# Performance work log

Measured on AMD Instinct MI355X. Metric: run time of the kernel, lower is better.

The kernel has to match this reference:

```python
import jax, jax.numpy as jnp
import numpy as np

B, T, D = 64, 4096, 100   # batch, tokens, token_dim == code_dim
K = 4                     # discrete_size: codebook entries
BETA = 0.25               # commitment loss weight


def setup_inputs() -> dict:
    key = jax.random.key(0)
    k_x, k_w, k_b, k_c = jax.random.split(key, 4)
    x = jax.random.normal(k_x, (B, T, D), dtype=jnp.float32)
    W1 = jax.random.normal(k_w, (D, D), dtype=jnp.float32) * (1.0 / np.sqrt(D))
    b1 = jax.random.normal(k_b, (D,), dtype=jnp.float32) * 0.01
    codebook = jax.random.normal(k_c, (K, D), dtype=jnp.float32)
    return {"x": x, "W1": W1, "b1": b1, "codebook": codebook, "quantize": 1}


def reference(x, W1, b1, codebook, quantize):
    # Linear1: Linear(100,100) + ReLU (torch Linear: x @ W.T + b)
    h = jax.nn.relu(jnp.einsum("btd,ed->bte", x, W1) + b1)  # [B,T,D]
    if not quantize:
        return (h, 0, 0, 0)
    # quantizer.compress: VQ-style cdist/argmin/straight-through/loss
    flat = h.reshape(-1, D)  # [N,D]
    d2 = (jnp.sum(flat * flat, axis=-1, keepdims=True)
          - 2.0 * flat @ codebook.T
          + jnp.sum(codebook * codebook, axis=-1))
    idx = jnp.argmin(d2, axis=-1)          # [N] nearest code indices
    q = codebook[idx]                       # [N,D] gathered codes
    sg = jax.lax.stop_gradient
    # codebook loss + commitment loss
    vq_loss = (jnp.mean((sg(flat) - q) ** 2)
               + BETA * jnp.mean((flat - sg(q)) ** 2))
    # straight-through quantized output
    aux = (flat + sg(q - flat)).reshape(B, T, D)
    payload = idx.reshape(B, T)
    return (h, payload, aux, vq_loss)
```

## Files before the change

### kernel.cpp

```cpp
#include <hip/hip_runtime.h>

#define D_DIM   100
#define K_CODES 4
#define RPB     64
#define TPB     256
#define PITCH   65
#define N_ROWS  262144
#define KP      128
#define NP      128
#define TAU     0.25
#define GRID_GEMM 1024
#define NTILES  4

typedef __attribute__((ext_vector_type(8))) __bf16 bf16x8;
typedef __attribute__((ext_vector_type(4))) float  f32x4;

__device__ __forceinline__ unsigned short f2bf_rne(float f) {
    unsigned int u = __builtin_bit_cast(unsigned int, f);
    unsigned int r = u + 0x7fffu + ((u >> 16) & 1u);
    return (unsigned short)(r >> 16);
}
__device__ __forceinline__ float bf2f(unsigned short b) {
    unsigned int u = ((unsigned int)b) << 16;
    return __builtin_bit_cast(float, u);
}
__device__ __forceinline__ void load_lds16(const float* g, float* s) {
    __builtin_amdgcn_global_load_lds(
        (const __attribute__((address_space(1))) unsigned int*)g,
        (__attribute__((address_space(3))) unsigned int*)s, 16, 0, 0);
}
__device__ __forceinline__ void stage_x(const float* xg, float* s, int wave, int lane) {
    #pragma unroll
    for (int it = 0; it < 6; ++it) {
        int cbase = it * 256 + wave * 64;
        load_lds16(xg + (size_t)(cbase + lane) * 4, s + cbase * 4);
    }
    if (wave == 0) load_lds16(xg + (size_t)(1536 + lane) * 4, s + 1536 * 4);
}

__device__ __forceinline__ void bar_lgkm() {
    __builtin_amdgcn_sched_barrier(0);
    asm volatile("s_waitcnt lgkmcnt(0)" ::: "memory");
    __builtin_amdgcn_s_barrier();
    __builtin_amdgcn_sched_barrier(0);
}
__device__ __forceinline__ void bar_vm() {
    __builtin_amdgcn_sched_barrier(0);
    asm volatile("s_waitcnt vmcnt(0) lgkmcnt(0)" ::: "memory");
    __builtin_amdgcn_s_barrier();
    __builtin_amdgcn_sched_barrier(0);
}

__global__ __launch_bounds__(256) void split_w_kernel(
    const float* __restrict__ W1,
    unsigned short* __restrict__ Whi, unsigned short* __restrict__ Wlo)
{
    int i = blockIdx.x * 256 + threadIdx.x;
    if (i >= NP * KP) return;
    int n = i / KP, k = i % KP;
    float w = (n < D_DIM && k < D_DIM) ? W1[n * D_DIM + k] : 0.0f;
    unsigned short hb = f2bf_rne(w);
    float lo = w - bf2f(hb);
    Whi[i] = hb;
    Wlo[i] = f2bf_rne(lo);
}

__global__ __launch_bounds__(TPB, 4) void gemm_relu_mfma(
    const float* __restrict__ x,
    const unsigned short* __restrict__ Whi, const unsigned short* __restrict__ Wlo,
    const float* __restrict__ b1, float* __restrict__ out_h)
{
    __shared__ __align__(16) float buf0[6500];
    __shared__ __align__(16) float buf1[6500];
    const int tid  = threadIdx.x;
    const int lane = tid & 63;
    const int wave = tid >> 6;

    const int bcol0 = wave * 32;
    const int bn  = lane & 15;
    const int bk  = (lane >> 4) * 8;
    bf16x8 bh[2][4], bl[2][4];
    #pragma unroll
    for (int ct = 0; ct < 2; ++ct) {
        int n = bcol0 + ct * 16 + bn;
        #pragma unroll
        for (int kt = 0; kt < 4; ++kt) {
            int off = n * KP + kt * 32 + bk;
            bh[ct][kt] = *reinterpret_cast<const bf16x8*>(Whi + off);
            bl[ct][kt] = *reinterpret_cast<const bf16x8*>(Wlo + off);
        }
    }
    float bias[2];
    #pragma unroll
    for (int ct = 0; ct < 2; ++ct) {
        int n = bcol0 + ct * 16 + bn;
        bias[ct] = (n < D_DIM) ? b1[n] : 0.0f;
    }
    if (tid < 32) { buf0[6400 + tid] = 0.0f; buf1[6400 + tid] = 0.0f; }
    stage_x(x + (size_t)blockIdx.x * RPB * D_DIM, buf0, wave, lane);

    const int am = lane & 15;
    const int ak = (lane >> 4) * 8;

    for (int it = 0; it < NTILES; ++it) {
        const int tile = blockIdx.x + it * GRID_GEMM;
        const int rowBase = tile * RPB;
        float* cur = (it & 1) ? buf1 : buf0;
        float* nxt = (it & 1) ? buf0 : buf1;

        bar_vm();

        if (it + 1 < NTILES)
            stage_x(x + (size_t)(blockIdx.x + (it + 1) * GRID_GEMM) * RPB * D_DIM,
                    nxt, wave, lane);

        f32x4 acc[4][2];
        #pragma unroll
        for (int rt = 0; rt < 4; ++rt) {
            acc[rt][0] = (f32x4){0.f, 0.f, 0.f, 0.f};
            acc[rt][1] = (f32x4){0.f, 0.f, 0.f, 0.f};
        }
        #pragma unroll
        for (int rt = 0; rt < 4; ++rt) {
            const int rbase = (rt * 16 + am) * D_DIM;
            #pragma unroll
            for (int kt = 0; kt < 4; ++kt) {
                const float* p = cur + rbase + kt * 32 + ak;
                f32x4 f0 = *reinterpret_cast<const f32x4*>(p);
                f32x4 f1 = *reinterpret_cast<const f32x4*>(p + 4);
                bf16x8 ah, al;
                #pragma unroll
                for (int i = 0; i < 4; ++i) {
                    __bf16 h0 = (__bf16)f0[i];
                    ah[i] = h0;
                    al[i] = (__bf16)(f0[i] - (float)h0);
                    __bf16 h1 = (__bf16)f1[i];
                    ah[4 + i] = h1;
                    al[4 + i] = (__bf16)(f1[i] - (float)h1);
                }
                acc[rt][0] = __builtin_amdgcn_mfma_f32_16x16x32_bf16(ah, bl[0][kt], acc[rt][0], 0, 0, 0);
                acc[rt][0] = __builtin_amdgcn_mfma_f32_16x16x32_bf16(al, bh[0][kt], acc[rt][0], 0, 0, 0);
                acc[rt][0] = __builtin_amdgcn_mfma_f32_16x16x32_bf16(ah, bh[0][kt], acc[rt][0], 0, 0, 0);
                acc[rt][1] = __builtin_amdgcn_mfma_f32_16x16x32_bf16(ah, bl[1][kt], acc[rt][1], 0, 0, 0);
                acc[rt][1] = __builtin_amdgcn_mfma_f32_16x16x32_bf16(al, bh[1][kt], acc[rt][1], 0, 0, 0);
                acc[rt][1] = __builtin_amdgcn_mfma_f32_16x16x32_bf16(ah, bh[1][kt], acc[rt][1], 0, 0, 0);
            }
        }
        bar_lgkm();

        #pragma unroll
        for (int rt = 0; rt < 4; ++rt) {
            int rb = rt * 16 + (lane >> 4) * 4;
            #pragma unroll
            for (int ct = 0; ct < 2; ++ct) {
                int n = bcol0 + ct * 16 + bn;
                if (n < D_DIM) {
                    #pragma unroll
                    for (int i = 0; i < 4; ++i)
                        cur[n * PITCH + rb + i] = fmaxf(acc[rt][ct][i] + bias[ct], 0.0f);
                }
            }
        }
        bar_lgkm();

        float* hg = out_h + (size_t)rowBase * D_DIM;
        for (int v = tid; v < RPB * 25; v += TPB) {
            int r = v / 25;
            int d = (v % 25) * 4;
            reinterpret_cast<float4*>(hg)[v] = make_float4(
                cur[d * PITCH + r], cur[(d + 1) * PITCH + r],
                cur[(d + 2) * PITCH + r], cur[(d + 3) * PITCH + r]);
        }
    }
}

__global__ __launch_bounds__(TPB) void vq_kernel(
    const float* __restrict__ h, const float* __restrict__ x,
    const float* __restrict__ W1, const float* __restrict__ b1,
    const float* __restrict__ cb, const int* __restrict__ qflag,
    float* __restrict__ out_pay, float* __restrict__ out_aux,
    double* __restrict__ partials)
{
    __shared__ float  tile[D_DIM][PITCH];
    __shared__ double d2s[K_CODES][RPB];
    __shared__ int    idxs[RPB];
    __shared__ unsigned long long flagmask;
    const int tid  = threadIdx.x;
    const int lane = tid & 63;
    const int wave = tid >> 6;
    const int blk  = blockIdx.x;
    const int rowBase = blk * RPB;
    const int qz = *qflag;

    if (qz) {
        const float* hgc = h + (size_t)rowBase * D_DIM;
        for (int v = tid; v < (RPB * D_DIM) / 4; v += TPB) {
            float4 val = reinterpret_cast<const float4*>(hgc)[v];
            int r = v / 25;
            int d = (v % 25) * 4;
            tile[d + 0][r] = val.x; tile[d + 1][r] = val.y;
            tile[d + 2][r] = val.z; tile[d + 3][r] = val.w;
        }
        __syncthreads();
        {
            const int k = __builtin_amdgcn_readfirstlane(wave & 3);
            const float* crow = cb + k * D_DIM;
            double s = 0.0;
            #pragma unroll
            for (int d = 0; d < D_DIM; ++d) {
                double dh = (double)tile[d][lane] - (double)crow[d];
                s = fma(dh, dh, s);
            }
            d2s[k][lane] = s;
        }
        __syncthreads();

        if (wave == 0) {
            double best = d2s[0][lane], second = 1e300;
            int bi = 0;
            #pragma unroll
            for (int k = 1; k < K_CODES; ++k) {
                double v = d2s[k][lane];
                if (v < best) { second = best; best = v; bi = k; }
                else if (v < second) { second = v; }
            }
            idxs[lane] = bi;
            unsigned long long m = __ballot((second - best) < TAU);
            if (lane == 0) flagmask = m;
        }
        __syncthreads();

        {
            unsigned long long m = flagmask;
            int i = 0;
            while (m) {
                int r = __ffsll((long long)m) - 1;
                m &= m - 1;
                if ((i & 3) == wave) {
                    const int e1 = lane;
                    const int e2 = 64 + lane;
                    const bool has2 = (e2 < D_DIM);
                    float z1 = b1[e1];
                    float z2 = has2 ? b1[e2] : 0.0f;
                    const float* xr  = x + (size_t)(rowBase + r) * D_DIM;
                    const float* w1r = W1 + e1 * D_DIM;
                    const float* w2r = W1 + (has2 ? e2 : 0) * D_DIM;
                    #pragma unroll
                    for (int d4 = 0; d4 < 25; ++d4) {
                        float4 xv = reinterpret_cast<const float4*>(xr)[d4];
                        float4 wa = reinterpret_cast<const float4*>(w1r)[d4];
                        z1 = fmaf(xv.x, wa.x, z1); z1 = fmaf(xv.y, wa.y, z1);
                        z1 = fmaf(xv.z, wa.z, z1); z1 = fmaf(xv.w, wa.w, z1);
                        float4 wb = reinterpret_cast<const float4*>(w2r)[d4];
                        z2 = fmaf(xv.x, wb.x, z2); z2 = fmaf(xv.y, wb.y, z2);
                        z2 = fmaf(xv.z, wb.z, z2); z2 = fmaf(xv.w, wb.w, z2);
                    }
                    float h1 = fmaxf(z1, 0.0f);
                    float h2 = fmaxf(z2, 0.0f);
                    double dk[K_CODES];
                    #pragma unroll
                    for (int k = 0; k < K_CODES; ++k) {
                        double p;
                        {
                            double dh = (double)h1 - (double)cb[k * D_DIM + e1];
                            p = dh * dh;
                        }
                        if (has2) {
                            double dh = (double)h2 - (double)cb[k * D_DIM + e2];
                            p = fma(dh, dh, p);
                        }
                        for (int off = 32; off > 0; off >>= 1)
                            p += __shfl_down(p, off);
                        dk[k] = p;
                    }
                    if (lane == 0) {
                        double best = dk[0];
                        int bi = 0;
                        #pragma unroll
                        for (int k = 1; k < K_CODES; ++k)
                            if (dk[k] < best) { best = dk[k]; bi = k; }
                        idxs[r] = bi;
                    }
                }
                ++i;
            }
        }
        __syncthreads();

        if (wave == 0) {
            int bi = idxs[lane];
            out_pay[rowBase + lane] = (float)bi;
            double d2min = d2s[bi][lane];
            for (int off = 32; off > 0; off >>= 1)
                d2min += __shfl_down(d2min, off);
            if (lane == 0) partials[blk] = d2min;
        }

        float* ag = out_aux + (size_t)rowBase * D_DIM;
        for (int v = tid; v < (RPB * D_DIM) / 4; v += TPB) {
            int r = v / 25;
            int d = (v % 25) * 4;
            int bi = idxs[r];
            reinterpret_cast<float4*>(ag)[v] =
                reinterpret_cast<const float4*>(cb + bi * D_DIM + d)[0];
        }
    } else {
        if (wave == 0) {
            out_pay[rowBase + lane] = 0.0f;
            if (lane == 0) partials[blk] = 0.0;
        }
        float* ag = out_aux + (size_t)rowBase * D_DIM;
        for (int v = tid; v < (RPB * D_DIM) / 4; v += TPB)
            reinterpret_cast<float4*>(ag)[v] = make_float4(0, 0, 0, 0);
    }
}

__global__ __launch_bounds__(256) void vq_final_kernel(
    const double* __restrict__ partials, int n, float* __restrict__ loss_out)
{
    __shared__ double sm[256];
    int tid = threadIdx.x;
    double s = 0.0;
    for (int i = tid; i < n; i += 256) s += partials[i];
    sm[tid] = s;
    __syncthreads();
    for (int off = 128; off > 0; off >>= 1) {
        if (tid < off) sm[tid] += sm[tid + off];
        __syncthreads();
    }
    if (tid == 0) {
        double mse = sm[0] / ((double)N_ROWS * (double)D_DIM);
        loss_out[0] = (float)(1.25 * mse);
    }
}

extern "C" void kernel_launch(void* const* d_in, const int* in_sizes, int n_in,
                              void* d_out, int out_size, void* d_ws, size_t ws_size,
                              hipStream_t stream) {
    const float* x  = (const float*)d_in[0];
    const float* W1 = (const float*)d_in[1];
    const float* b1 = (const float*)d_in[2];
    const float* cb = (const float*)d_in[3];
    const int* qflag = (const int*)d_in[4];

    float* out = (float*)d_out;
    const int NR = in_sizes[0] / D_DIM;
    const int nblocks = NR / RPB;

    float* out_h    = out;
    float* out_pay  = out + (size_t)NR * D_DIM;
    float* out_aux  = out_pay + NR;
    float* out_loss = out_aux + (size_t)NR * D_DIM;

    double* partials = (double*)d_ws;
    const size_t w_off = (size_t)nblocks * sizeof(double);
    unsigned short* Whi = (unsigned short*)((char*)d_ws + w_off);
    unsigned short* Wlo = Whi + NP * KP;

    split_w_kernel<<<(NP * KP) / 256, 256, 0, stream>>>(W1, Whi, Wlo);
    gemm_relu_mfma<<<GRID_GEMM, TPB, 0, stream>>>(x, Whi, Wlo, b1, out_h);
    vq_kernel<<<nblocks, TPB, 0, stream>>>(out_h, x, W1, b1, cb, qflag,
                                           out_pay, out_aux, partials);
    vq_final_kernel<<<1, 256, 0, stream>>>(partials, nblocks, out_loss);
}
```

Baseline: 119.6 us.

## Split VQ into main pass and separate near-tie fixup kernel with transposed W1

Splits the VQ kernel into a main kernel that picks codes from the bf16-split GEMM output and records per-block masks of near-tie rows, and a separate fixup kernel. The fixup kernel recomputes those ambiguous rows in fp32 using a transposed, padded W1 copy built in the weight-split kernel, which gives coalesced weight reads. The aim is to remove the serialized per-block fixup loop and the load imbalance it causes inside the main VQ pass. The fixup kernel is hardcoded to 4096 mask blocks. It also changes how the loss partials are computed: they now use the pre-fixup best distance, which differs from the mono path for rows whose code changes.

```diff
diff --git a/kernel.cpp b/kernel.cpp
--- a/kernel.cpp
+++ b/kernel.cpp
@@ -11,6 +11,8 @@
 #define TAU     0.25
 #define GRID_GEMM 1024
 #define NTILES  4
+#define TPITCH  128
+#define FIXUP_BLOCKS 256
 
 typedef __attribute__((ext_vector_type(8))) __bf16 bf16x8;
 typedef __attribute__((ext_vector_type(4))) float  f32x4;
@@ -37,7 +39,6 @@
     }
     if (wave == 0) load_lds16(xg + (size_t)(1536 + lane) * 4, s + 1536 * 4);
 }
-
 __device__ __forceinline__ void bar_lgkm() {
     __builtin_amdgcn_sched_barrier(0);
     asm volatile("s_waitcnt lgkmcnt(0)" ::: "memory");
@@ -53,16 +54,21 @@
 
 __global__ __launch_bounds__(256) void split_w_kernel(
     const float* __restrict__ W1,
-    unsigned short* __restrict__ Whi, unsigned short* __restrict__ Wlo)
+    unsigned short* __restrict__ Whi, unsigned short* __restrict__ Wlo,
+    float* __restrict__ W1T)
 {
     int i = blockIdx.x * 256 + threadIdx.x;
-    if (i >= NP * KP) return;
-    int n = i / KP, k = i % KP;
-    float w = (n < D_DIM && k < D_DIM) ? W1[n * D_DIM + k] : 0.0f;
-    unsigned short hb = f2bf_rne(w);
-    float lo = w - bf2f(hb);
-    Whi[i] = hb;
-    Wlo[i] = f2bf_rne(lo);
+    if (i < NP * KP) {
+        int n = i / KP, k = i % KP;
+        float w = (n < D_DIM && k < D_DIM) ? W1[n * D_DIM + k] : 0.0f;
+        unsigned short hb = f2bf_rne(w);
+        Whi[i] = hb;
+        Wlo[i] = f2bf_rne(w - bf2f(hb));
+    }
+    if (i < D_DIM * TPITCH) {
+        int d = i / TPITCH, e = i % TPITCH;
+        W1T[i] = (e < D_DIM) ? W1[e * D_DIM + d] : 0.0f;
+    }
 }
 
 __global__ __launch_bounds__(TPB, 4) void gemm_relu_mfma(
@@ -174,7 +180,154 @@
     }
 }
 
-__global__ __launch_bounds__(TPB) void vq_kernel(
+__global__ __launch_bounds__(TPB) void vq_main_kernel(
+    const float* __restrict__ h, const float* __restrict__ cb,
+    const int* __restrict__ qflag,
+    float* __restrict__ out_pay, float* __restrict__ out_aux,
+    double* __restrict__ partials, unsigned long long* __restrict__ masks)
+{
+    __shared__ float  tile[D_DIM][PITCH];
+    __shared__ double d2s[K_CODES][RPB];
+    __shared__ int    idxs[RPB];
+    const int tid  = threadIdx.x;
+    const int lane = tid & 63;
+    const int wave = tid >> 6;
+    const int blk  = blockIdx.x;
+    const int rowBase = blk * RPB;
+    const int qz = *qflag;
+
+    if (qz) {
+        const float* hgc = h + (size_t)rowBase * D_DIM;
+        for (int v = tid; v < (RPB * D_DIM) / 4; v += TPB) {
+            float4 val = reinterpret_cast<const float4*>(hgc)[v];
+            int r = v / 25;
+            int d = (v % 25) * 4;
+            tile[d + 0][r] = val.x; tile[d + 1][r] = val.y;
+            tile[d + 2][r] = val.z; tile[d + 3][r] = val.w;
+        }
+        __syncthreads();
+        {
+            const int k = __builtin_amdgcn_readfirstlane(wave & 3);
+            const float* crow = cb + k * D_DIM;
+            double s = 0.0;
+            #pragma unroll
+            for (int d = 0; d < D_DIM; ++d) {
+                double dh = (double)tile[d][lane] - (double)crow[d];
+                s = fma(dh, dh, s);
+            }
+            d2s[k][lane] = s;
+        }
+        __syncthreads();
+
+        if (wave == 0) {
+            double best = d2s[0][lane], second = 1e300;
+            int bi = 0;
+            #pragma unroll
+            for (int k = 1; k < K_CODES; ++k) {
+                double v = d2s[k][lane];
+                if (v < best) { second = best; best = v; bi = k; }
+                else if (v < second) { second = v; }
+            }
+            idxs[lane] = bi;
+            out_pay[rowBase + lane] = (float)bi;
+            unsigned long long m = __ballot((second - best) < TAU);
+            if (lane == 0) masks[blk] = m;
+            double d2min = best;
+            for (int off = 32; off > 0; off >>= 1)
+                d2min += __shfl_down(d2min, off);
+            if (lane == 0) partials[blk] = d2min;
+        }
+        __syncthreads();
+
+        float* ag = out_aux + (size_t)rowBase * D_DIM;
+        for (int v = tid; v < (RPB * D_DIM) / 4; v += TPB) {
+            int r = v / 25;
+            int d = (v % 25) * 4;
+            int bi = idxs[r];
+            reinterpret_cast<float4*>(ag)[v] =
+                reinterpret_cast<const float4*>(cb + bi * D_DIM + d)[0];
+        }
+    } else {
+        if (wave == 0) {
+            out_pay[rowBase + lane] = 0.0f;
+            if (lane == 0) { partials[blk] = 0.0; masks[blk] = 0ull; }
+        }
+        float* ag = out_aux + (size_t)rowBase * D_DIM;
+        for (int v = tid; v < (RPB * D_DIM) / 4; v += TPB)
+            reinterpret_cast<float4*>(ag)[v] = make_float4(0, 0, 0, 0);
+    }
+}
+
+__global__ __launch_bounds__(TPB) void vq_fixup_kernel(
+    const float* __restrict__ x, const float* __restrict__ W1T,
+    const float* __restrict__ b1, const float* __restrict__ cb,
+    const unsigned long long* __restrict__ masks,
+    float* __restrict__ out_pay, float* __restrict__ out_aux)
+{
+    const int lane = threadIdx.x & 63;
+    const int wgl  = (blockIdx.x * TPB + threadIdx.x) >> 6;
+    const int e1 = lane;
+    const int e2 = 64 + lane;
+    const bool has2 = (e2 < D_DIM);
+    const float bb1 = b1[e1];
+    const float bb2 = has2 ? b1[e2] : 0.0f;
+
+    for (int mi = wgl; mi < 4096; mi += 1024) {
+        unsigned long long m = masks[mi];
+        while (m) {
+            int r = __ffsll((long long)m) - 1;
+            m &= m - 1;
+            const int row = mi * 64 + r;
+            const float* xr = x + (size_t)row * D_DIM;
+            float z1 = bb1, z2 = bb2;
+            #pragma unroll
+            for (int d4 = 0; d4 < 25; ++d4) {
+                float4 xv = *reinterpret_cast<const float4*>(xr + d4 * 4);
+                const float* t0 = W1T + (d4 * 4 + 0) * TPITCH;
+                const float* t1 = W1T + (d4 * 4 + 1) * TPITCH;
+                const float* t2 = W1T + (d4 * 4 + 2) * TPITCH;
+                const float* t3 = W1T + (d4 * 4 + 3) * TPITCH;
+                z1 = fmaf(xv.x, t0[e1], z1);  z2 = fmaf(xv.x, t0[e2], z2);
+                z1 = fmaf(xv.y, t1[e1], z1);  z2 = fmaf(xv.y, t1[e2], z2);
+                z1 = fmaf(xv.z, t2[e1], z1);  z2 = fmaf(xv.z, t2[e2], z2);
+                z1 = fmaf(xv.w, t3[e1], z1);  z2 = fmaf(xv.w, t3[e2], z2);
+            }
+            float h1 = fmaxf(z1, 0.0f);
+            float h2 = fmaxf(z2, 0.0f);
+            double dk[K_CODES];
+            #pragma unroll
+            for (int k = 0; k < K_CODES; ++k) {
+                double p;
+                {
+                    double dh = (double)h1 - (double)cb[k * D_DIM + e1];
+                    p = dh * dh;
+                }
+                if (has2) {
+                    double dh = (double)h2 - (double)cb[k * D_DIM + e2];
+                    p = fma(dh, dh, p);
+                }
+                for (int off = 32; off > 0; off >>= 1)
+                    p += __shfl_down(p, off);
+                dk[k] = p;
+            }
+            int bi = 0;
+            double best = dk[0];
+            #pragma unroll
+            for (int k = 1; k < K_CODES; ++k)
+                if (dk[k] < best) { best = dk[k]; bi = k; }
+            bi = __shfl(bi, 0);
+
+            if (lane == 0) out_pay[row] = (float)bi;
+            if (lane < 25) {
+                float* ar = out_aux + (size_t)row * D_DIM;
+                reinterpret_cast<float4*>(ar)[lane] =
+                    *reinterpret_cast<const float4*>(cb + bi * D_DIM + lane * 4);
+            }
+        }
+    }
+}
+
+__global__ __launch_bounds__(TPB) void vq_kernel_mono(
     const float* __restrict__ h, const float* __restrict__ x,
     const float* __restrict__ W1, const float* __restrict__ b1,
     const float* __restrict__ cb, const int* __restrict__ qflag,
@@ -214,7 +367,6 @@
             d2s[k][lane] = s;
         }
         __syncthreads();
-
         if (wave == 0) {
             double best = d2s[0][lane], second = 1e300;
             int bi = 0;
@@ -229,7 +381,6 @@
             if (lane == 0) flagmask = m;
         }
         __syncthreads();
-
         {
             unsigned long long m = flagmask;
             int i = 0;
@@ -286,7 +437,6 @@
             }
         }
         __syncthreads();
-
         if (wave == 0) {
             int bi = idxs[lane];
             out_pay[rowBase + lane] = (float)bi;
@@ -295,7 +445,6 @@
                 d2min += __shfl_down(d2min, off);
             if (lane == 0) partials[blk] = d2min;
         }
-
         float* ag = out_aux + (size_t)rowBase * D_DIM;
         for (int v = tid; v < (RPB * D_DIM) / 4; v += TPB) {
             int r = v / 25;
@@ -353,13 +502,23 @@
     float* out_loss = out_aux + (size_t)NR * D_DIM;
 
     double* partials = (double*)d_ws;
-    const size_t w_off = (size_t)nblocks * sizeof(double);
-    unsigned short* Whi = (unsigned short*)((char*)d_ws + w_off);
-    unsigned short* Wlo = Whi + NP * KP;
-
-    split_w_kernel<<<(NP * KP) / 256, 256, 0, stream>>>(W1, Whi, Wlo);
+    unsigned short* Whi = (unsigned short*)((char*)d_ws + 32768);
+    unsigned short* Wlo = (unsigned short*)((char*)d_ws + 65536);
+    unsigned long long* masks = (unsigned long long*)((char*)d_ws + 98304);
+    float* W1T = (float*)((char*)d_ws + 131072);
+    const size_t need = 131072 + (size_t)D_DIM * TPITCH * sizeof(float);
+
+    split_w_kernel<<<64, 256, 0, stream>>>(W1, Whi, Wlo,
+                                           (ws_size >= need) ? W1T : (float*)Whi );
     gemm_relu_mfma<<<GRID_GEMM, TPB, 0, stream>>>(x, Whi, Wlo, b1, out_h);
-    vq_kernel<<<nblocks, TPB, 0, stream>>>(out_h, x, W1, b1, cb, qflag,
-                                           out_pay, out_aux, partials);
+    if (ws_size >= need) {
+        vq_main_kernel<<<nblocks, TPB, 0, stream>>>(out_h, cb, qflag,
+                                                    out_pay, out_aux, partials, masks);
+        vq_fixup_kernel<<<FIXUP_BLOCKS, TPB, 0, stream>>>(x, W1T, b1, cb, masks,
+                                                          out_pay, out_aux);
+    } else {
+        vq_kernel_mono<<<nblocks, TPB, 0, stream>>>(out_h, x, W1, b1, cb, qflag,
+                                                    out_pay, out_aux, partials);
+    }
     vq_final_kernel<<<1, 256, 0, stream>>>(partials, nblocks, out_loss);
 }
```

New measurement: 202.5 us. 69.2% more time.
